# Optimization experiments

Hardware: AMD Instinct MI355X
Metric: run time of the kernel (lower is better)

## Reference

```python
import jax, jax.numpy as jnp
import numpy as np

B, H, S, D = 4, 8, 2048, 64

def setup_inputs() -> dict:
    key = jax.random.key(0)
    k1, k2 = jax.random.split(key)
    q = jax.random.normal(k1, (B, H, S, D), dtype=jnp.float32)
    kv = jax.random.normal(k2, (B, H, S, D), dtype=jnp.float32)
    mask = jnp.zeros((1, 1, S, S), dtype=jnp.float32)
    return {"q": q, "kv": kv, "mask": mask}

def reference(q, kv, mask):
    # score = q @ kv^T / sqrt(d_k) + mask ; softmax over last dim ; @ kv
    d_k = jnp.asarray(kv.shape[-1], dtype=q.dtype)
    score = jnp.einsum('bhqd,bhkd->bhqk', q, kv) / jnp.sqrt(d_k)
    score = score + mask
    attn = jax.nn.softmax(score, axis=-1)
    out = jnp.einsum('bhqk,bhkd->bhqd', attn, kv)
    return out
```

## Files before the change

kernel.cpp:

```cpp
#include <hip/hip_runtime.h>
#include <hip/hip_bf16.h>
#include <stdint.h>


typedef __bf16 bf16;
typedef __attribute__((ext_vector_type(8))) __bf16 bf16x8;
typedef __attribute__((ext_vector_type(4))) __bf16 bf16x4;
typedef __attribute__((ext_vector_type(4))) float floatx4;

#define SLEN 2048
#define DH   64
#define BR   64
#define BC   64
#define NKT  (SLEN / BC)
#define NQT  (SLEN / BR)
#define BH_N 32
#define LOG2E 1.44269504088896341f

#define CHB_L  1024
#define IMGB_L 8192
#define IMGE_G 4096

#define AS1 __attribute__((address_space(1)))
#define AS3 __attribute__((address_space(3)))

static __device__ inline void gload_lds16(const void* g, void* l) {
    __builtin_amdgcn_global_load_lds((const AS1 uint32_t*)g, (AS3 uint32_t*)l, 16, 0, 0);
}

static_assert(BH_N == NQT, "prep kernel folds bh and qt onto one grid axis");

static __device__ inline int phys_key(int l) {
    int h = l >> 5, l5 = l & 31, q = l5 >> 3, j = l5 & 7;
    return 32 * h + (j < 4 ? 4 * q + j : 16 + 4 * q + (j - 4));
}

__global__ __launch_bounds__(256) void kv_prep(
    const float* __restrict__ kv, const float* __restrict__ mask,
    bf16* __restrict__ kvK, bf16* __restrict__ kvT, int* __restrict__ flags)
{
    __shared__ bf16 Tl[64 * 72];
    __shared__ int wany[4];
    const int kt = blockIdx.x, z = blockIdx.y;
    const int t = threadIdx.x;

    float acc = 0.f;
#pragma unroll
    for (int i = 0; i < 4; ++i) {
        int f = i * 256 + t;
        int row = f >> 4, c4 = (f & 15) * 4;
        const float4 v = *(const float4*)(mask + (size_t)(z * BR + row) * SLEN + kt * BC + c4);
        acc = fmaxf(acc, fmaxf(fmaxf(fabsf(v.x), fabsf(v.y)), fmaxf(fabsf(v.z), fabsf(v.w))));
    }
    unsigned long long any = __ballot(acc != 0.f);
    if ((t & 63) == 0) wany[t >> 6] = (any != 0ull) ? 1 : 0;

    const float* src = kv + ((size_t)z * SLEN + kt * BC) * DH;
#pragma unroll
    for (int i = 0; i < 4; ++i) {
        int f = i * 256 + t;
        int key = f >> 4, d4 = (f & 15) * 4;
        float4 v = *(const float4*)(src + (size_t)key * DH + d4);
        bf16x4 b; b[0] = (bf16)v.x; b[1] = (bf16)v.y; b[2] = (bf16)v.z; b[3] = (bf16)v.w;
        *(bf16x4*)&Tl[key * 72 + d4] = b;
    }
    __syncthreads();
    if (t == 0) flags[z * NKT + kt] = wany[0] | wany[1] | wany[2] | wany[3];

    bf16* outK = kvK + ((size_t)z * NKT + kt) * IMGE_G;
#pragma unroll
    for (int i = 0; i < 2; ++i) {
        int G = i * 256 + t;
        int c = G >> 6, L = G & 63, rl = L >> 3, p = L & 7;
        int g = (p - rl - 4 * (c & 1)) & 7, key = 8 * c + rl;
        bf16x8 w = *(const bf16x8*)&Tl[key * 72 + g * 8];
        *(bf16x8*)(outK + (size_t)G * 8) = w;
    }
    bf16* outV = kvT + ((size_t)z * NKT + kt) * IMGE_G;
#pragma unroll
    for (int i = 0; i < 2; ++i) {
        int G = i * 256 + t;
        int c = G >> 6, L = G & 63, dl = L >> 3, p = L & 7;
        int g = (p - dl - 4 * (c & 1)) & 7, d = 8 * c + dl;
        bf16x8 w;
#pragma unroll
        for (int j = 0; j < 8; ++j)
            w[j] = Tl[phys_key(8 * g + j) * 72 + d];
        *(bf16x8*)(outV + (size_t)G * 8) = w;
    }
}

__global__ __launch_bounds__(1024) void attn_fwd10(
    const float* __restrict__ q, const float* __restrict__ mask,
    const int* __restrict__ flags,
    const bf16* __restrict__ kvK, const bf16* __restrict__ kvT,
    float* __restrict__ out)
{
    __shared__ __align__(16) char smem[65536];

    const int bh = blockIdx.x;
    const int qt = blockIdx.y;
    const int q0 = qt * 128;
    const int t = threadIdx.x;
    const int wave = t >> 6, lane = t & 63;
    const int grp = wave >> 3;
    const int w8 = wave & 7;
    const int ln16 = lane & 15, quad = lane >> 4;
    const int ln8 = ln16 & 7, hb = ln16 >> 3;

    const float qscale = 0.125f * LOG2E;
    bf16x8 aq[2];
    {
        const float* qrow = q + ((size_t)bh * SLEN + q0 + w8 * 16 + ln16) * DH;
#pragma unroll
        for (int kc = 0; kc < 2; ++kc) {
            float4 f0 = *(const float4*)(qrow + kc * 32 + quad * 8);
            float4 f1 = *(const float4*)(qrow + kc * 32 + quad * 8 + 4);
            bf16x8 a;
            a[0] = (bf16)(f0.x * qscale); a[1] = (bf16)(f0.y * qscale);
            a[2] = (bf16)(f0.z * qscale); a[3] = (bf16)(f0.w * qscale);
            a[4] = (bf16)(f1.x * qscale); a[5] = (bf16)(f1.y * qscale);
            a[6] = (bf16)(f1.z * qscale); a[7] = (bf16)(f1.w * qscale);
            aq[kc] = a;
        }
    }

    const int fqt = qt * 2 + (w8 >> 2);
    unsigned fmask;
    {
        int ld = (lane < 32) ? flags[fqt * NKT + lane] : 0;
        fmask = (unsigned)__ballot(ld != 0);
    }

    const int kbase0 = hb * CHB_L + ln8 * 128 + (((quad + ln8 + 4 * hb) & 7) << 4);
    const int kbase1 = hb * CHB_L + ln8 * 128 + (((quad + 4 + ln8 + 4 * hb) & 7) << 4);

    floatx4 o[4];
#pragma unroll
    for (int dt = 0; dt < 4; ++dt) o[dt] = (floatx4){0.f, 0.f, 0.f, 0.f};
    float m_run = -3.0e38f, l_run = 0.f;

    const bf16* kvKb = kvK + (size_t)bh * NKT * IMGE_G;
    const bf16* kvTb = kvT + (size_t)bh * NKT * IMGE_G;
    const int kt0 = grp * (NKT / 2);
    char* Gb = smem + grp * 32768;

    {
        const bf16* sK = kvKb + (size_t)kt0 * IMGE_G;
        const bf16* sV = kvTb + (size_t)kt0 * IMGE_G;
        gload_lds16(sK + (size_t)w8 * 512 + lane * 8, Gb + w8 * CHB_L);
        gload_lds16(sV + (size_t)w8 * 512 + lane * 8, Gb + IMGB_L + w8 * CHB_L);
    }

    for (int e = 0; e < NKT / 2; ++e) {
        __syncthreads();
        const int kt = kt0 + e;

        if (e + 1 < NKT / 2) {
            char* Bn = Gb + ((e + 1) & 1) * 16384;
            const bf16* sK = kvKb + (size_t)(kt + 1) * IMGE_G;
            const bf16* sV = kvTb + (size_t)(kt + 1) * IMGE_G;
            gload_lds16(sK + (size_t)w8 * 512 + lane * 8, Bn + w8 * CHB_L);
            gload_lds16(sV + (size_t)w8 * 512 + lane * 8, Bn + IMGB_L + w8 * CHB_L);
        }

        const char* Kb = Gb + (e & 1) * 16384;
        const char* Vb = Kb + IMGB_L;

        floatx4 s[4];
#pragma unroll
        for (int nt = 0; nt < 4; ++nt) {
            bf16x8 a0 = *(const bf16x8*)(Kb + nt * 2048 + kbase0);
            bf16x8 a1 = *(const bf16x8*)(Kb + nt * 2048 + kbase1);
            floatx4 acc = (floatx4){0.f, 0.f, 0.f, 0.f};
            acc = __builtin_amdgcn_mfma_f32_16x16x32_bf16(a0, aq[0], acc, 0, 0, 0);
            acc = __builtin_amdgcn_mfma_f32_16x16x32_bf16(a1, aq[1], acc, 0, 0, 0);
            s[nt] = acc;
        }

        if (fmask & (1u << kt)) {
            const float* mrow = mask + (size_t)(q0 + w8 * 16 + ln16) * SLEN + kt * BC;
#pragma unroll
            for (int nt = 0; nt < 4; ++nt) {
                float4 mv = *(const float4*)(mrow + 16 * nt + quad * 4);
                s[nt][0] += mv.x * LOG2E; s[nt][1] += mv.y * LOG2E;
                s[nt][2] += mv.z * LOG2E; s[nt][3] += mv.w * LOG2E;
            }
        }

        float t01 = fmaxf(fmaxf(s[0][0], s[0][1]), fmaxf(s[0][2], s[0][3]));
        float t23 = fmaxf(fmaxf(s[1][0], s[1][1]), fmaxf(s[1][2], s[1][3]));
        float t45 = fmaxf(fmaxf(s[2][0], s[2][1]), fmaxf(s[2][2], s[2][3]));
        float t67 = fmaxf(fmaxf(s[3][0], s[3][1]), fmaxf(s[3][2], s[3][3]));
        float tmax = fmaxf(fmaxf(t01, t23), fmaxf(t45, t67));
        tmax = fmaxf(tmax, __shfl_xor(tmax, 16));
        tmax = fmaxf(tmax, __shfl_xor(tmax, 32));
        float mnew = fmaxf(m_run, tmax);
        unsigned long long grew = __ballot(mnew > m_run);
        float alpha = exp2f(m_run - mnew);
        m_run = mnew;

        float rs = 0.f;
        bf16x8 pf0, pf1;
#pragma unroll
        for (int r = 0; r < 4; ++r) {
            float p0 = exp2f(s[0][r] - mnew);
            float p1 = exp2f(s[1][r] - mnew);
            float p2 = exp2f(s[2][r] - mnew);
            float p3 = exp2f(s[3][r] - mnew);
            rs += (p0 + p1) + (p2 + p3);
            pf0[r] = (bf16)p0; pf0[4 + r] = (bf16)p1;
            pf1[r] = (bf16)p2; pf1[4 + r] = (bf16)p3;
        }
        rs += __shfl_xor(rs, 16);
        rs += __shfl_xor(rs, 32);

        if (grew) {
            l_run = l_run * alpha + rs;
            float a0 = __shfl(alpha, quad * 4 + 0);
            float a1 = __shfl(alpha, quad * 4 + 1);
            float a2 = __shfl(alpha, quad * 4 + 2);
            float a3 = __shfl(alpha, quad * 4 + 3);
#pragma unroll
            for (int dt = 0; dt < 4; ++dt) {
                o[dt][0] *= a0; o[dt][1] *= a1; o[dt][2] *= a2; o[dt][3] *= a3;
            }
        } else {
            l_run += rs;
        }

#pragma unroll
        for (int dt = 0; dt < 4; ++dt) {
            bf16x8 v0 = *(const bf16x8*)(Vb + dt * 2048 + kbase0);
            bf16x8 v1 = *(const bf16x8*)(Vb + dt * 2048 + kbase1);
            o[dt] = __builtin_amdgcn_mfma_f32_16x16x32_bf16(pf0, v0, o[dt], 0, 0, 0);
            o[dt] = __builtin_amdgcn_mfma_f32_16x16x32_bf16(pf1, v1, o[dt], 0, 0, 0);
        }
    }

    __syncthreads();
    float* Xo  = (float*)smem;
    float* Xml = (float*)(smem + 32768);

    if (grp == 1) {
        float* xo = Xo + (size_t)w8 * 16 * 64;
#pragma unroll
        for (int dt = 0; dt < 4; ++dt) {
            int col = ln16 + 16 * dt;
            xo[(quad * 4 + 0) * 64 + col] = o[dt][0];
            xo[(quad * 4 + 1) * 64 + col] = o[dt][1];
            xo[(quad * 4 + 2) * 64 + col] = o[dt][2];
            xo[(quad * 4 + 3) * 64 + col] = o[dt][3];
        }
        Xml[(w8 * 16 + ln16) * 2 + 0] = m_run;
        Xml[(w8 * 16 + ln16) * 2 + 1] = l_run;
    }
    __syncthreads();
    if (grp == 0) {
        const float* xo = Xo + (size_t)w8 * 16 * 64;
        float* ob = out + ((size_t)bh * SLEN + q0 + w8 * 16) * DH;
#pragma unroll
        for (int r = 0; r < 4; ++r) {
            int row = quad * 4 + r;
            float m0 = __shfl(m_run, row);
            float l0 = __shfl(l_run, row);
            float m1 = Xml[(w8 * 16 + row) * 2 + 0];
            float l1 = Xml[(w8 * 16 + row) * 2 + 1];
            float M  = fmaxf(m0, m1);
            float a0 = exp2f(m0 - M), a1 = exp2f(m1 - M);
            float inv = 1.f / (l0 * a0 + l1 * a1);
#pragma unroll
            for (int dt = 0; dt < 4; ++dt) {
                int col = ln16 + 16 * dt;
                ob[row * DH + col] = (o[dt][r] * a0 + xo[row * 64 + col] * a1) * inv;
            }
        }
    }
}

#define LDT 72
__global__ __launch_bounds__(256) void attn_mask_flags(
    const float* __restrict__ mask, int* __restrict__ flags)
{
    const int kt = blockIdx.x, qt = blockIdx.y;
    const int t = threadIdx.x;
    float acc = 0.f;
#pragma unroll
    for (int i = 0; i < 4; ++i) {
        int f = i * 256 + t;
        int row = f >> 4, c4 = (f & 15) * 4;
        const float4 v = *(const float4*)(mask + (size_t)(qt * BR + row) * SLEN + kt * BC + c4);
        acc = fmaxf(acc, fmaxf(fmaxf(fabsf(v.x), fabsf(v.y)), fmaxf(fabsf(v.z), fabsf(v.w))));
    }
    unsigned long long any = __ballot(acc != 0.f);
    __shared__ int wany[4];
    if ((t & 63) == 0) wany[t >> 6] = (any != 0ull) ? 1 : 0;
    __syncthreads();
    if (t == 0) flags[qt * NKT + kt] = wany[0] | wany[1] | wany[2] | wany[3];
}

__global__ __launch_bounds__(256) void attn_fwd(
    const float* __restrict__ q, const float* __restrict__ kv,
    const float* __restrict__ mask, const int* __restrict__ flags,
    float* __restrict__ out)
{
    __shared__ __align__(16) bf16 Kl[BC * LDT];
    __shared__ __align__(16) bf16 Vt[DH * LDT];
    __shared__ __align__(16) bf16 Pl[BR * LDT];

    const int qt = blockIdx.x;
    const int bh = blockIdx.y;
    const int q0 = qt * BR;
    const int t = threadIdx.x;
    const int wave = t >> 6, lane = t & 63;
    const int ln16 = lane & 15, quad = lane >> 4;

    const float qscale = 0.125f * LOG2E;
    bf16x8 aq[2];
    {
        const float* qrow = q + ((size_t)bh * SLEN + q0 + wave * 16 + ln16) * DH;
#pragma unroll
        for (int kc = 0; kc < 2; ++kc) {
            float4 f0 = *(const float4*)(qrow + kc * 32 + quad * 8);
            float4 f1 = *(const float4*)(qrow + kc * 32 + quad * 8 + 4);
            bf16x8 a;
            a[0] = (bf16)(f0.x * qscale); a[1] = (bf16)(f0.y * qscale);
            a[2] = (bf16)(f0.z * qscale); a[3] = (bf16)(f0.w * qscale);
            a[4] = (bf16)(f1.x * qscale); a[5] = (bf16)(f1.y * qscale);
            a[6] = (bf16)(f1.z * qscale); a[7] = (bf16)(f1.w * qscale);
            aq[kc] = a;
        }
    }

    floatx4 o[4];
#pragma unroll
    for (int dt = 0; dt < 4; ++dt) o[dt] = (floatx4){0.f, 0.f, 0.f, 0.f};
    float m_run[4], l_run[4];
#pragma unroll
    for (int r = 0; r < 4; ++r) { m_run[r] = -3.0e38f; l_run[r] = 0.f; }

    const float* kvb = kv + (size_t)bh * SLEN * DH;

    for (int kt = 0; kt < NKT; ++kt) {
        float4 st[4];
        const float* kvt = kvb + (size_t)kt * BC * DH;
#pragma unroll
        for (int i = 0; i < 4; ++i) {
            int f = i * 256 + t;
            st[i] = *(const float4*)(kvt + (size_t)f * 4);
        }
        __syncthreads();
#pragma unroll
        for (int i = 0; i < 4; ++i) {
            int f = i * 256 + t;
            int key = f >> 4, d4 = (f & 15) * 4;
            bf16 b0 = (bf16)st[i].x, b1 = (bf16)st[i].y, b2 = (bf16)st[i].z, b3 = (bf16)st[i].w;
            *(bf16x4*)&Kl[key * LDT + d4] = (bf16x4){b0, b1, b2, b3};
            Vt[(d4 + 0) * LDT + key] = b0;
            Vt[(d4 + 1) * LDT + key] = b1;
            Vt[(d4 + 2) * LDT + key] = b2;
            Vt[(d4 + 3) * LDT + key] = b3;
        }
        __syncthreads();

        floatx4 s[4];
#pragma unroll
        for (int nt = 0; nt < 4; ++nt) {
            s[nt] = (floatx4){0.f, 0.f, 0.f, 0.f};
#pragma unroll
            for (int kc = 0; kc < 2; ++kc) {
                bf16x8 bk = *(const bf16x8*)&Kl[(ln16 + 16 * nt) * LDT + kc * 32 + quad * 8];
                s[nt] = __builtin_amdgcn_mfma_f32_16x16x32_bf16(aq[kc], bk, s[nt], 0, 0, 0);
            }
        }

        if (!flags || flags[qt * NKT + kt]) {
            const float* mrow = mask + (size_t)(q0 + quad * 4) * SLEN + kt * BC + ln16;
#pragma unroll
            for (int r = 0; r < 4; ++r)
#pragma unroll
                for (int nt = 0; nt < 4; ++nt)
                    s[nt][r] += mrow[(size_t)r * SLEN + nt * 16] * LOG2E;
        }

#pragma unroll
        for (int r = 0; r < 4; ++r) {
            float mx = fmaxf(fmaxf(s[0][r], s[1][r]), fmaxf(s[2][r], s[3][r]));
            mx = fmaxf(mx, __shfl_xor(mx, 1));
            mx = fmaxf(mx, __shfl_xor(mx, 2));
            mx = fmaxf(mx, __shfl_xor(mx, 4));
            mx = fmaxf(mx, __shfl_xor(mx, 8));
            float mnew = fmaxf(m_run[r], mx);
            float alpha = exp2f(m_run[r] - mnew);
            m_run[r] = mnew;
            float rs = 0.f;
#pragma unroll
            for (int nt = 0; nt < 4; ++nt) {
                float p = exp2f(s[nt][r] - mnew);
                s[nt][r] = p;
                rs += p;
            }
            rs += __shfl_xor(rs, 1);
            rs += __shfl_xor(rs, 2);
            rs += __shfl_xor(rs, 4);
            rs += __shfl_xor(rs, 8);
            l_run[r] = l_run[r] * alpha + rs;
#pragma unroll
            for (int dt = 0; dt < 4; ++dt) o[dt][r] *= alpha;
        }

#pragma unroll
        for (int nt = 0; nt < 4; ++nt)
#pragma unroll
            for (int r = 0; r < 4; ++r)
                Pl[(wave * 16 + quad * 4 + r) * LDT + ln16 + 16 * nt] = (bf16)s[nt][r];

#pragma unroll
        for (int kc2 = 0; kc2 < 2; ++kc2) {
            bf16x8 pfr = *(const bf16x8*)&Pl[(wave * 16 + ln16) * LDT + kc2 * 32 + quad * 8];
#pragma unroll
            for (int dt = 0; dt < 4; ++dt) {
                bf16x8 vfr = *(const bf16x8*)&Vt[(ln16 + 16 * dt) * LDT + kc2 * 32 + quad * 8];
                o[dt] = __builtin_amdgcn_mfma_f32_16x16x32_bf16(pfr, vfr, o[dt], 0, 0, 0);
            }
        }
    }

#pragma unroll
    for (int r = 0; r < 4; ++r) {
        float inv = 1.0f / l_run[r];
        int qrow = q0 + wave * 16 + quad * 4 + r;
        float* orow = out + ((size_t)bh * SLEN + qrow) * DH;
#pragma unroll
        for (int dt = 0; dt < 4; ++dt)
            orow[ln16 + 16 * dt] = o[dt][r] * inv;
    }
}

extern "C" void kernel_launch(void* const* d_in, const int* in_sizes, int n_in,
                              void* d_out, int out_size, void* d_ws, size_t ws_size,
                              hipStream_t stream)
{
    const float* q    = (const float*)d_in[0];
    const float* kv   = (const float*)d_in[1];
    const float* mask = (const float*)d_in[2];
    float* out = (float*)d_out;

    const size_t kvKoff = 4096;
    const size_t kvToff = kvKoff + (size_t)BH_N * NKT * IMGE_G * 2;
    const size_t need   = kvToff + (size_t)BH_N * NKT * IMGE_G * 2;

    if (ws_size >= need) {
        int*  flags = (int*)d_ws;
        bf16* kvK   = (bf16*)((char*)d_ws + kvKoff);
        bf16* kvT   = (bf16*)((char*)d_ws + kvToff);
        kv_prep<<<dim3(NKT, BH_N), 256, 0, stream>>>(kv, mask, kvK, kvT, flags);
        attn_fwd10<<<dim3(BH_N, SLEN / 128), 1024, 0, stream>>>(q, mask, flags, kvK, kvT, out);
    } else {
        int* flags = nullptr;
        if (ws_size >= (size_t)NQT * NKT * sizeof(int)) {
            flags = (int*)d_ws;
            attn_mask_flags<<<dim3(NKT, NQT), 256, 0, stream>>>(mask, flags);
        }
        attn_fwd<<<dim3(NQT, BH_N), 256, 0, stream>>>(q, kv, mask, flags, out);
    }
}
```

Measured before the change: 165.6 us.

## Switch attention kernel to 32x32x16 MFMA tiles with 512-thread blocks

Rewrites the main attention kernel to use 32x32x16 bf16 MFMA instructions, so each wave owns 32 query rows instead of 16, and halves the block to 512 threads. The V-transpose layout in the prep kernel is changed to match the new operand fragment ordering. Larger MFMA tiles reduce the LDS fragment loads and instructions per FLOP and cut the cross-lane reductions for row max and sum. The cost is more accumulator registers per wave, fewer waves per block for latency hiding, and more complex per-row alpha shuffles and mask gathers.

```diff
diff --git a/kernel.cpp b/kernel.cpp
--- a/kernel.cpp
+++ b/kernel.cpp
@@ -7,6 +7,7 @@
 typedef __attribute__((ext_vector_type(8))) __bf16 bf16x8;
 typedef __attribute__((ext_vector_type(4))) __bf16 bf16x4;
 typedef __attribute__((ext_vector_type(4))) float floatx4;
+typedef __attribute__((ext_vector_type(16))) float floatx16;
 
 #define SLEN 2048
 #define DH   64
@@ -18,7 +19,6 @@
 #define LOG2E 1.44269504088896341f
 
 #define CHB_L  1024
-#define IMGB_L 8192
 #define IMGE_G 4096
 
 #define AS1 __attribute__((address_space(1)))
@@ -30,9 +30,9 @@
 
 static_assert(BH_N == NQT, "prep kernel folds bh and qt onto one grid axis");
 
-static __device__ inline int phys_key(int l) {
-    int h = l >> 5, l5 = l & 31, q = l5 >> 3, j = l5 & 7;
-    return 32 * h + (j < 4 ? 4 * q + j : 16 + 4 * q + (j - 4));
+static __device__ inline int phys_key32(int l) {
+    int kc = l >> 4, rem = l & 15, h = rem >> 3, j = rem & 7;
+    return 16 * kc + 4 * h + j + 4 * (j >> 2);
 }
 
 __global__ __launch_bounds__(256) void kv_prep(
@@ -85,12 +85,12 @@
         bf16x8 w;
 #pragma unroll
         for (int j = 0; j < 8; ++j)
-            w[j] = Tl[phys_key(8 * g + j) * 72 + d];
+            w[j] = Tl[phys_key32(8 * g + j) * 72 + d];
         *(bf16x8*)(outV + (size_t)G * 8) = w;
     }
 }
 
-__global__ __launch_bounds__(1024) void attn_fwd10(
+__global__ __launch_bounds__(512) void attn_fwd11(
     const float* __restrict__ q, const float* __restrict__ mask,
     const int* __restrict__ flags,
     const bf16* __restrict__ kvK, const bf16* __restrict__ kvT,
@@ -103,19 +103,26 @@
     const int q0 = qt * 128;
     const int t = threadIdx.x;
     const int wave = t >> 6, lane = t & 63;
-    const int grp = wave >> 3;
-    const int w8 = wave & 7;
-    const int ln16 = lane & 15, quad = lane >> 4;
-    const int ln8 = ln16 & 7, hb = ln16 >> 3;
+    const int grp = wave >> 2;
+    const int w4 = wave & 3;
+    const int l31 = lane & 31, h = lane >> 5;
+
+    const int laneRow = (l31 >> 3) * 1024 + (l31 & 7) * 128;
+    const int c0 = (l31 & 7) + 4 * ((l31 >> 3) & 1) + h;
+    const int pos0 = ((0 + c0) & 7) * 16;
+    const int pos1 = ((2 + c0) & 7) * 16;
+    const int pos2 = ((4 + c0) & 7) * 16;
+    const int pos3 = ((6 + c0) & 7) * 16;
 
     const float qscale = 0.125f * LOG2E;
-    bf16x8 aq[2];
+    bf16x8 aq[4];
     {
-        const float* qrow = q + ((size_t)bh * SLEN + q0 + w8 * 16 + ln16) * DH;
-#pragma unroll
-        for (int kc = 0; kc < 2; ++kc) {
-            float4 f0 = *(const float4*)(qrow + kc * 32 + quad * 8);
-            float4 f1 = *(const float4*)(qrow + kc * 32 + quad * 8 + 4);
+        const float* qrow = q + ((size_t)bh * SLEN + q0 + w4 * 32 + l31) * DH;
+#pragma unroll
+        for (int kc = 0; kc < 4; ++kc) {
+            int d0 = 16 * kc + 8 * h;
+            float4 f0 = *(const float4*)(qrow + d0);
+            float4 f1 = *(const float4*)(qrow + d0 + 4);
             bf16x8 a;
             a[0] = (bf16)(f0.x * qscale); a[1] = (bf16)(f0.y * qscale);
             a[2] = (bf16)(f0.z * qscale); a[3] = (bf16)(f0.w * qscale);
@@ -125,19 +132,16 @@
         }
     }
 
-    const int fqt = qt * 2 + (w8 >> 2);
+    const int fqt = qt * 2 + (w4 >> 1);
     unsigned fmask;
     {
         int ld = (lane < 32) ? flags[fqt * NKT + lane] : 0;
         fmask = (unsigned)__ballot(ld != 0);
     }
 
-    const int kbase0 = hb * CHB_L + ln8 * 128 + (((quad + ln8 + 4 * hb) & 7) << 4);
-    const int kbase1 = hb * CHB_L + ln8 * 128 + (((quad + 4 + ln8 + 4 * hb) & 7) << 4);
-
-    floatx4 o[4];
-#pragma unroll
-    for (int dt = 0; dt < 4; ++dt) o[dt] = (floatx4){0.f, 0.f, 0.f, 0.f};
+    floatx16 o0, o1;
+#pragma unroll
+    for (int i = 0; i < 16; ++i) { o0[i] = 0.f; o1[i] = 0.f; }
     float m_run = -3.0e38f, l_run = 0.f;
 
     const bf16* kvKb = kvK + (size_t)bh * NKT * IMGE_G;
@@ -148,8 +152,10 @@
     {
         const bf16* sK = kvKb + (size_t)kt0 * IMGE_G;
         const bf16* sV = kvTb + (size_t)kt0 * IMGE_G;
-        gload_lds16(sK + (size_t)w8 * 512 + lane * 8, Gb + w8 * CHB_L);
-        gload_lds16(sV + (size_t)w8 * 512 + lane * 8, Gb + IMGB_L + w8 * CHB_L);
+        gload_lds16(sK + (size_t)(2 * w4) * 512 + lane * 8,     Gb + (2 * w4) * CHB_L);
+        gload_lds16(sK + (size_t)(2 * w4 + 1) * 512 + lane * 8, Gb + (2 * w4 + 1) * CHB_L);
+        gload_lds16(sV + (size_t)(2 * w4) * 512 + lane * 8,     Gb + 8192 + (2 * w4) * CHB_L);
+        gload_lds16(sV + (size_t)(2 * w4 + 1) * 512 + lane * 8, Gb + 8192 + (2 * w4 + 1) * CHB_L);
     }
 
     for (int e = 0; e < NKT / 2; ++e) {
@@ -160,40 +166,52 @@
             char* Bn = Gb + ((e + 1) & 1) * 16384;
             const bf16* sK = kvKb + (size_t)(kt + 1) * IMGE_G;
             const bf16* sV = kvTb + (size_t)(kt + 1) * IMGE_G;
-            gload_lds16(sK + (size_t)w8 * 512 + lane * 8, Bn + w8 * CHB_L);
-            gload_lds16(sV + (size_t)w8 * 512 + lane * 8, Bn + IMGB_L + w8 * CHB_L);
+            gload_lds16(sK + (size_t)(2 * w4) * 512 + lane * 8,     Bn + (2 * w4) * CHB_L);
+            gload_lds16(sK + (size_t)(2 * w4 + 1) * 512 + lane * 8, Bn + (2 * w4 + 1) * CHB_L);
+            gload_lds16(sV + (size_t)(2 * w4) * 512 + lane * 8,     Bn + 8192 + (2 * w4) * CHB_L);
+            gload_lds16(sV + (size_t)(2 * w4 + 1) * 512 + lane * 8, Bn + 8192 + (2 * w4 + 1) * CHB_L);
         }
 
         const char* Kb = Gb + (e & 1) * 16384;
-        const char* Vb = Kb + IMGB_L;
-
-        floatx4 s[4];
-#pragma unroll
-        for (int nt = 0; nt < 4; ++nt) {
-            bf16x8 a0 = *(const bf16x8*)(Kb + nt * 2048 + kbase0);
-            bf16x8 a1 = *(const bf16x8*)(Kb + nt * 2048 + kbase1);
-            floatx4 acc = (floatx4){0.f, 0.f, 0.f, 0.f};
-            acc = __builtin_amdgcn_mfma_f32_16x16x32_bf16(a0, aq[0], acc, 0, 0, 0);
-            acc = __builtin_amdgcn_mfma_f32_16x16x32_bf16(a1, aq[1], acc, 0, 0, 0);
-            s[nt] = acc;
+        const char* Vb = Kb + 8192;
+
+        floatx16 s0, s1;
+#pragma unroll
+        for (int i = 0; i < 16; ++i) { s0[i] = 0.f; s1[i] = 0.f; }
+        {
+            bf16x8 k00 = *(const bf16x8*)(Kb + laneRow + pos0);
+            bf16x8 k10 = *(const bf16x8*)(Kb + 4096 + laneRow + pos0);
+            s0 = __builtin_amdgcn_mfma_f32_32x32x16_bf16(k00, aq[0], s0, 0, 0, 0);
+            s1 = __builtin_amdgcn_mfma_f32_32x32x16_bf16(k10, aq[0], s1, 0, 0, 0);
+            bf16x8 k01 = *(const bf16x8*)(Kb + laneRow + pos1);
+            bf16x8 k11 = *(const bf16x8*)(Kb + 4096 + laneRow + pos1);
+            s0 = __builtin_amdgcn_mfma_f32_32x32x16_bf16(k01, aq[1], s0, 0, 0, 0);
+            s1 = __builtin_amdgcn_mfma_f32_32x32x16_bf16(k11, aq[1], s1, 0, 0, 0);
+            bf16x8 k02 = *(const bf16x8*)(Kb + laneRow + pos2);
+            bf16x8 k12 = *(const bf16x8*)(Kb + 4096 + laneRow + pos2);
+            s0 = __builtin_amdgcn_mfma_f32_32x32x16_bf16(k02, aq[2], s0, 0, 0, 0);
+            s1 = __builtin_amdgcn_mfma_f32_32x32x16_bf16(k12, aq[2], s1, 0, 0, 0);
+            bf16x8 k03 = *(const bf16x8*)(Kb + laneRow + pos3);
+            bf16x8 k13 = *(const bf16x8*)(Kb + 4096 + laneRow + pos3);
+            s0 = __builtin_amdgcn_mfma_f32_32x32x16_bf16(k03, aq[3], s0, 0, 0, 0);
+            s1 = __builtin_amdgcn_mfma_f32_32x32x16_bf16(k13, aq[3], s1, 0, 0, 0);
         }
 
         if (fmask & (1u << kt)) {
-            const float* mrow = mask + (size_t)(q0 + w8 * 16 + ln16) * SLEN + kt * BC;
-#pragma unroll
-            for (int nt = 0; nt < 4; ++nt) {
-                float4 mv = *(const float4*)(mrow + 16 * nt + quad * 4);
-                s[nt][0] += mv.x * LOG2E; s[nt][1] += mv.y * LOG2E;
-                s[nt][2] += mv.z * LOG2E; s[nt][3] += mv.w * LOG2E;
-            }
-        }
-
-        float t01 = fmaxf(fmaxf(s[0][0], s[0][1]), fmaxf(s[0][2], s[0][3]));
-        float t23 = fmaxf(fmaxf(s[1][0], s[1][1]), fmaxf(s[1][2], s[1][3]));
-        float t45 = fmaxf(fmaxf(s[2][0], s[2][1]), fmaxf(s[2][2], s[2][3]));
-        float t67 = fmaxf(fmaxf(s[3][0], s[3][1]), fmaxf(s[3][2], s[3][3]));
-        float tmax = fmaxf(fmaxf(t01, t23), fmaxf(t45, t67));
-        tmax = fmaxf(tmax, __shfl_xor(tmax, 16));
+            const float* mrow = mask + (size_t)(q0 + w4 * 32 + l31) * SLEN + kt * BC;
+#pragma unroll
+            for (int r = 0; r < 16; ++r) {
+                int key = (r & 3) + 8 * (r >> 2) + 4 * h;
+                s0[r] += mrow[key] * LOG2E;
+                s1[r] += mrow[32 + key] * LOG2E;
+            }
+        }
+
+        float tmax = s0[0];
+#pragma unroll
+        for (int r = 1; r < 16; ++r) tmax = fmaxf(tmax, s0[r]);
+#pragma unroll
+        for (int r = 0; r < 16; ++r) tmax = fmaxf(tmax, s1[r]);
         tmax = fmaxf(tmax, __shfl_xor(tmax, 32));
         float mnew = fmaxf(m_run, tmax);
         unsigned long long grew = __ballot(mnew > m_run);
@@ -201,40 +219,49 @@
         m_run = mnew;
 
         float rs = 0.f;
-        bf16x8 pf0, pf1;
-#pragma unroll
-        for (int r = 0; r < 4; ++r) {
-            float p0 = exp2f(s[0][r] - mnew);
-            float p1 = exp2f(s[1][r] - mnew);
-            float p2 = exp2f(s[2][r] - mnew);
-            float p3 = exp2f(s[3][r] - mnew);
-            rs += (p0 + p1) + (p2 + p3);
-            pf0[r] = (bf16)p0; pf0[4 + r] = (bf16)p1;
-            pf1[r] = (bf16)p2; pf1[4 + r] = (bf16)p3;
-        }
-        rs += __shfl_xor(rs, 16);
+        bf16x8 pf[4];
+#pragma unroll
+        for (int kcb = 0; kcb < 2; ++kcb) {
+#pragma unroll
+            for (int j = 0; j < 8; ++j) {
+                float p0 = exp2f(s0[8 * kcb + j] - mnew);
+                float p1 = exp2f(s1[8 * kcb + j] - mnew);
+                rs += p0 + p1;
+                pf[kcb][j] = (bf16)p0;
+                pf[2 + kcb][j] = (bf16)p1;
+            }
+        }
         rs += __shfl_xor(rs, 32);
 
         if (grew) {
             l_run = l_run * alpha + rs;
-            float a0 = __shfl(alpha, quad * 4 + 0);
-            float a1 = __shfl(alpha, quad * 4 + 1);
-            float a2 = __shfl(alpha, quad * 4 + 2);
-            float a3 = __shfl(alpha, quad * 4 + 3);
-#pragma unroll
-            for (int dt = 0; dt < 4; ++dt) {
-                o[dt][0] *= a0; o[dt][1] *= a1; o[dt][2] *= a2; o[dt][3] *= a3;
+#pragma unroll
+            for (int r = 0; r < 16; ++r) {
+                int R = (r & 3) + 8 * (r >> 2) + 4 * h;
+                float ar = __shfl(alpha, R);
+                o0[r] *= ar; o1[r] *= ar;
             }
         } else {
             l_run += rs;
         }
 
-#pragma unroll
-        for (int dt = 0; dt < 4; ++dt) {
-            bf16x8 v0 = *(const bf16x8*)(Vb + dt * 2048 + kbase0);
-            bf16x8 v1 = *(const bf16x8*)(Vb + dt * 2048 + kbase1);
-            o[dt] = __builtin_amdgcn_mfma_f32_16x16x32_bf16(pf0, v0, o[dt], 0, 0, 0);
-            o[dt] = __builtin_amdgcn_mfma_f32_16x16x32_bf16(pf1, v1, o[dt], 0, 0, 0);
+        {
+            bf16x8 v00 = *(const bf16x8*)(Vb + laneRow + pos0);
+            bf16x8 v10 = *(const bf16x8*)(Vb + 4096 + laneRow + pos0);
+            o0 = __builtin_amdgcn_mfma_f32_32x32x16_bf16(pf[0], v00, o0, 0, 0, 0);
+            o1 = __builtin_amdgcn_mfma_f32_32x32x16_bf16(pf[0], v10, o1, 0, 0, 0);
+            bf16x8 v01 = *(const bf16x8*)(Vb + laneRow + pos1);
+            bf16x8 v11 = *(const bf16x8*)(Vb + 4096 + laneRow + pos1);
+            o0 = __builtin_amdgcn_mfma_f32_32x32x16_bf16(pf[1], v01, o0, 0, 0, 0);
+            o1 = __builtin_amdgcn_mfma_f32_32x32x16_bf16(pf[1], v11, o1, 0, 0, 0);
+            bf16x8 v02 = *(const bf16x8*)(Vb + laneRow + pos2);
+            bf16x8 v12 = *(const bf16x8*)(Vb + 4096 + laneRow + pos2);
+            o0 = __builtin_amdgcn_mfma_f32_32x32x16_bf16(pf[2], v02, o0, 0, 0, 0);
+            o1 = __builtin_amdgcn_mfma_f32_32x32x16_bf16(pf[2], v12, o1, 0, 0, 0);
+            bf16x8 v03 = *(const bf16x8*)(Vb + laneRow + pos3);
+            bf16x8 v13 = *(const bf16x8*)(Vb + 4096 + laneRow + pos3);
+            o0 = __builtin_amdgcn_mfma_f32_32x32x16_bf16(pf[3], v03, o0, 0, 0, 0);
+            o1 = __builtin_amdgcn_mfma_f32_32x32x16_bf16(pf[3], v13, o1, 0, 0, 0);
         }
     }
 
@@ -243,37 +270,30 @@
     float* Xml = (float*)(smem + 32768);
 
     if (grp == 1) {
-        float* xo = Xo + (size_t)w8 * 16 * 64;
-#pragma unroll
-        for (int dt = 0; dt < 4; ++dt) {
-            int col = ln16 + 16 * dt;
-            xo[(quad * 4 + 0) * 64 + col] = o[dt][0];
-            xo[(quad * 4 + 1) * 64 + col] = o[dt][1];
-            xo[(quad * 4 + 2) * 64 + col] = o[dt][2];
-            xo[(quad * 4 + 3) * 64 + col] = o[dt][3];
-        }
-        Xml[(w8 * 16 + ln16) * 2 + 0] = m_run;
-        Xml[(w8 * 16 + ln16) * 2 + 1] = l_run;
+#pragma unroll
+        for (int r = 0; r < 16; ++r) {
+            int row = w4 * 32 + (r & 3) + 8 * (r >> 2) + 4 * h;
+            Xo[row * 64 + l31]      = o0[r];
+            Xo[row * 64 + 32 + l31] = o1[r];
+        }
+        Xml[(w4 * 32 + l31) * 2 + 0] = m_run;
+        Xml[(w4 * 32 + l31) * 2 + 1] = l_run;
     }
     __syncthreads();
     if (grp == 0) {
-        const float* xo = Xo + (size_t)w8 * 16 * 64;
-        float* ob = out + ((size_t)bh * SLEN + q0 + w8 * 16) * DH;
-#pragma unroll
-        for (int r = 0; r < 4; ++r) {
-            int row = quad * 4 + r;
-            float m0 = __shfl(m_run, row);
-            float l0 = __shfl(l_run, row);
-            float m1 = Xml[(w8 * 16 + row) * 2 + 0];
-            float l1 = Xml[(w8 * 16 + row) * 2 + 1];
+        float* ob = out + ((size_t)bh * SLEN + q0 + w4 * 32) * DH;
+#pragma unroll
+        for (int r = 0; r < 16; ++r) {
+            int R = (r & 3) + 8 * (r >> 2) + 4 * h;
+            float m0 = __shfl(m_run, R);
+            float l0 = __shfl(l_run, R);
+            float m1 = Xml[(w4 * 32 + R) * 2 + 0];
+            float l1 = Xml[(w4 * 32 + R) * 2 + 1];
             float M  = fmaxf(m0, m1);
             float a0 = exp2f(m0 - M), a1 = exp2f(m1 - M);
             float inv = 1.f / (l0 * a0 + l1 * a1);
-#pragma unroll
-            for (int dt = 0; dt < 4; ++dt) {
-                int col = ln16 + 16 * dt;
-                ob[row * DH + col] = (o[dt][r] * a0 + xo[row * 64 + col] * a1) * inv;
-            }
+            ob[R * DH + l31]      = (o0[r] * a0 + Xo[(w4 * 32 + R) * 64 + l31]      * a1) * inv;
+            ob[R * DH + 32 + l31] = (o1[r] * a0 + Xo[(w4 * 32 + R) * 64 + 32 + l31] * a1) * inv;
         }
     }
 }
@@ -455,7 +475,7 @@
         bf16* kvK   = (bf16*)((char*)d_ws + kvKoff);
         bf16* kvT   = (bf16*)((char*)d_ws + kvToff);
         kv_prep<<<dim3(NKT, BH_N), 256, 0, stream>>>(kv, mask, kvK, kvT, flags);
-        attn_fwd10<<<dim3(BH_N, SLEN / 128), 1024, 0, stream>>>(q, mask, flags, kvK, kvT, out);
+        attn_fwd11<<<dim3(BH_N, SLEN / 128), 512, 0, stream>>>(q, mask, flags, kvK, kvT, out);
     } else {
         int* flags = nullptr;
         if (ws_size >= (size_t)NQT * NKT * sizeof(int)) {
```

New measurement: 166.4 us. About the same (+0.5%).

## Halve waves per block, give each wave two 16-row query tiles

Applied to the files above, without the earlier changes.

The attention kernel now launches 512 threads (8 waves, two groups of four) instead of 1024. Each wave processes two 16-row query slices, so every K/V fragment read from LDS feeds two MFMAs, halving LDS read traffic per unit of compute and interleaving independent MFMA chains. The exp2f calls are also swapped for the raw hardware exp2 builtin. The trade-off is more accumulator and score registers per wave and fewer waves per block to hide latency, with launch bounds asking for 4 blocks per CU.

```diff
diff --git a/kernel.cpp b/kernel.cpp
--- a/kernel.cpp
+++ b/kernel.cpp
@@ -18,7 +18,6 @@
 #define LOG2E 1.44269504088896341f
 
 #define CHB_L  1024
-#define IMGB_L 8192
 #define IMGE_G 4096
 
 #define AS1 __attribute__((address_space(1)))
@@ -26,6 +25,10 @@
 
 static __device__ inline void gload_lds16(const void* g, void* l) {
     __builtin_amdgcn_global_load_lds((const AS1 uint32_t*)g, (AS3 uint32_t*)l, 16, 0, 0);
+}
+
+static __device__ inline float fexp2(float x) {
+    return __builtin_amdgcn_exp2f(x);
 }
 
 static_assert(BH_N == NQT, "prep kernel folds bh and qt onto one grid axis");
@@ -90,7 +93,7 @@
     }
 }
 
-__global__ __launch_bounds__(1024) void attn_fwd10(
+__global__ __launch_bounds__(512, 4) void attn_fwd14(
     const float* __restrict__ q, const float* __restrict__ mask,
     const int* __restrict__ flags,
     const bf16* __restrict__ kvK, const bf16* __restrict__ kvT,
@@ -103,15 +106,16 @@
     const int q0 = qt * 128;
     const int t = threadIdx.x;
     const int wave = t >> 6, lane = t & 63;
-    const int grp = wave >> 3;
-    const int w8 = wave & 7;
+    const int grp = wave >> 2;
+    const int w4 = wave & 3;
     const int ln16 = lane & 15, quad = lane >> 4;
     const int ln8 = ln16 & 7, hb = ln16 >> 3;
 
     const float qscale = 0.125f * LOG2E;
-    bf16x8 aq[2];
-    {
-        const float* qrow = q + ((size_t)bh * SLEN + q0 + w8 * 16 + ln16) * DH;
+    bf16x8 aq[2][2];
+#pragma unroll
+    for (int rs = 0; rs < 2; ++rs) {
+        const float* qrow = q + ((size_t)bh * SLEN + q0 + w4 * 32 + rs * 16 + ln16) * DH;
 #pragma unroll
         for (int kc = 0; kc < 2; ++kc) {
             float4 f0 = *(const float4*)(qrow + kc * 32 + quad * 8);
@@ -121,11 +125,11 @@
             a[2] = (bf16)(f0.z * qscale); a[3] = (bf16)(f0.w * qscale);
             a[4] = (bf16)(f1.x * qscale); a[5] = (bf16)(f1.y * qscale);
             a[6] = (bf16)(f1.z * qscale); a[7] = (bf16)(f1.w * qscale);
-            aq[kc] = a;
-        }
-    }
-
-    const int fqt = qt * 2 + (w8 >> 2);
+            aq[rs][kc] = a;
+        }
+    }
+
+    const int fqt = qt * 2 + (w4 >> 1);
     unsigned fmask;
     {
         int ld = (lane < 32) ? flags[fqt * NKT + lane] : 0;
@@ -135,10 +139,12 @@
     const int kbase0 = hb * CHB_L + ln8 * 128 + (((quad + ln8 + 4 * hb) & 7) << 4);
     const int kbase1 = hb * CHB_L + ln8 * 128 + (((quad + 4 + ln8 + 4 * hb) & 7) << 4);
 
-    floatx4 o[4];
-#pragma unroll
-    for (int dt = 0; dt < 4; ++dt) o[dt] = (floatx4){0.f, 0.f, 0.f, 0.f};
-    float m_run = -3.0e38f, l_run = 0.f;
+    floatx4 o[2][4];
+#pragma unroll
+    for (int rs = 0; rs < 2; ++rs)
+#pragma unroll
+        for (int dt = 0; dt < 4; ++dt) o[rs][dt] = (floatx4){0.f, 0.f, 0.f, 0.f};
+    float m_run[2] = {-3.0e38f, -3.0e38f}, l_run[2] = {0.f, 0.f};
 
     const bf16* kvKb = kvK + (size_t)bh * NKT * IMGE_G;
     const bf16* kvTb = kvT + (size_t)bh * NKT * IMGE_G;
@@ -148,8 +154,10 @@
     {
         const bf16* sK = kvKb + (size_t)kt0 * IMGE_G;
         const bf16* sV = kvTb + (size_t)kt0 * IMGE_G;
-        gload_lds16(sK + (size_t)w8 * 512 + lane * 8, Gb + w8 * CHB_L);
-        gload_lds16(sV + (size_t)w8 * 512 + lane * 8, Gb + IMGB_L + w8 * CHB_L);
+        gload_lds16(sK + (size_t)(2 * w4) * 512 + lane * 8,     Gb + (2 * w4) * CHB_L);
+        gload_lds16(sK + (size_t)(2 * w4 + 1) * 512 + lane * 8, Gb + (2 * w4 + 1) * CHB_L);
+        gload_lds16(sV + (size_t)(2 * w4) * 512 + lane * 8,     Gb + 8192 + (2 * w4) * CHB_L);
+        gload_lds16(sV + (size_t)(2 * w4 + 1) * 512 + lane * 8, Gb + 8192 + (2 * w4 + 1) * CHB_L);
     }
 
     for (int e = 0; e < NKT / 2; ++e) {
@@ -160,81 +168,96 @@
             char* Bn = Gb + ((e + 1) & 1) * 16384;
             const bf16* sK = kvKb + (size_t)(kt + 1) * IMGE_G;
             const bf16* sV = kvTb + (size_t)(kt + 1) * IMGE_G;
-            gload_lds16(sK + (size_t)w8 * 512 + lane * 8, Bn + w8 * CHB_L);
-            gload_lds16(sV + (size_t)w8 * 512 + lane * 8, Bn + IMGB_L + w8 * CHB_L);
+            gload_lds16(sK + (size_t)(2 * w4) * 512 + lane * 8,     Bn + (2 * w4) * CHB_L);
+            gload_lds16(sK + (size_t)(2 * w4 + 1) * 512 + lane * 8, Bn + (2 * w4 + 1) * CHB_L);
+            gload_lds16(sV + (size_t)(2 * w4) * 512 + lane * 8,     Bn + 8192 + (2 * w4) * CHB_L);
+            gload_lds16(sV + (size_t)(2 * w4 + 1) * 512 + lane * 8, Bn + 8192 + (2 * w4 + 1) * CHB_L);
         }
 
         const char* Kb = Gb + (e & 1) * 16384;
-        const char* Vb = Kb + IMGB_L;
-
-        floatx4 s[4];
+        const char* Vb = Kb + 8192;
+
+        floatx4 s[2][4];
 #pragma unroll
         for (int nt = 0; nt < 4; ++nt) {
             bf16x8 a0 = *(const bf16x8*)(Kb + nt * 2048 + kbase0);
             bf16x8 a1 = *(const bf16x8*)(Kb + nt * 2048 + kbase1);
-            floatx4 acc = (floatx4){0.f, 0.f, 0.f, 0.f};
-            acc = __builtin_amdgcn_mfma_f32_16x16x32_bf16(a0, aq[0], acc, 0, 0, 0);
-            acc = __builtin_amdgcn_mfma_f32_16x16x32_bf16(a1, aq[1], acc, 0, 0, 0);
-            s[nt] = acc;
+            floatx4 accA = (floatx4){0.f, 0.f, 0.f, 0.f};
+            floatx4 accB = (floatx4){0.f, 0.f, 0.f, 0.f};
+            accA = __builtin_amdgcn_mfma_f32_16x16x32_bf16(a0, aq[0][0], accA, 0, 0, 0);
+            accB = __builtin_amdgcn_mfma_f32_16x16x32_bf16(a0, aq[1][0], accB, 0, 0, 0);
+            accA = __builtin_amdgcn_mfma_f32_16x16x32_bf16(a1, aq[0][1], accA, 0, 0, 0);
+            accB = __builtin_amdgcn_mfma_f32_16x16x32_bf16(a1, aq[1][1], accB, 0, 0, 0);
+            s[0][nt] = accA;
+            s[1][nt] = accB;
         }
 
         if (fmask & (1u << kt)) {
-            const float* mrow = mask + (size_t)(q0 + w8 * 16 + ln16) * SLEN + kt * BC;
-#pragma unroll
-            for (int nt = 0; nt < 4; ++nt) {
-                float4 mv = *(const float4*)(mrow + 16 * nt + quad * 4);
-                s[nt][0] += mv.x * LOG2E; s[nt][1] += mv.y * LOG2E;
-                s[nt][2] += mv.z * LOG2E; s[nt][3] += mv.w * LOG2E;
-            }
-        }
-
-        float t01 = fmaxf(fmaxf(s[0][0], s[0][1]), fmaxf(s[0][2], s[0][3]));
-        float t23 = fmaxf(fmaxf(s[1][0], s[1][1]), fmaxf(s[1][2], s[1][3]));
-        float t45 = fmaxf(fmaxf(s[2][0], s[2][1]), fmaxf(s[2][2], s[2][3]));
-        float t67 = fmaxf(fmaxf(s[3][0], s[3][1]), fmaxf(s[3][2], s[3][3]));
-        float tmax = fmaxf(fmaxf(t01, t23), fmaxf(t45, t67));
-        tmax = fmaxf(tmax, __shfl_xor(tmax, 16));
-        tmax = fmaxf(tmax, __shfl_xor(tmax, 32));
-        float mnew = fmaxf(m_run, tmax);
-        unsigned long long grew = __ballot(mnew > m_run);
-        float alpha = exp2f(m_run - mnew);
-        m_run = mnew;
-
-        float rs = 0.f;
-        bf16x8 pf0, pf1;
-#pragma unroll
-        for (int r = 0; r < 4; ++r) {
-            float p0 = exp2f(s[0][r] - mnew);
-            float p1 = exp2f(s[1][r] - mnew);
-            float p2 = exp2f(s[2][r] - mnew);
-            float p3 = exp2f(s[3][r] - mnew);
-            rs += (p0 + p1) + (p2 + p3);
-            pf0[r] = (bf16)p0; pf0[4 + r] = (bf16)p1;
-            pf1[r] = (bf16)p2; pf1[4 + r] = (bf16)p3;
-        }
-        rs += __shfl_xor(rs, 16);
-        rs += __shfl_xor(rs, 32);
-
-        if (grew) {
-            l_run = l_run * alpha + rs;
-            float a0 = __shfl(alpha, quad * 4 + 0);
-            float a1 = __shfl(alpha, quad * 4 + 1);
-            float a2 = __shfl(alpha, quad * 4 + 2);
-            float a3 = __shfl(alpha, quad * 4 + 3);
-#pragma unroll
-            for (int dt = 0; dt < 4; ++dt) {
-                o[dt][0] *= a0; o[dt][1] *= a1; o[dt][2] *= a2; o[dt][3] *= a3;
-            }
-        } else {
-            l_run += rs;
+#pragma unroll
+            for (int rs = 0; rs < 2; ++rs) {
+                const float* mrow = mask + (size_t)(q0 + w4 * 32 + rs * 16 + ln16) * SLEN + kt * BC;
+#pragma unroll
+                for (int nt = 0; nt < 4; ++nt) {
+                    float4 mv = *(const float4*)(mrow + 16 * nt + quad * 4);
+                    s[rs][nt][0] += mv.x * LOG2E; s[rs][nt][1] += mv.y * LOG2E;
+                    s[rs][nt][2] += mv.z * LOG2E; s[rs][nt][3] += mv.w * LOG2E;
+                }
+            }
+        }
+
+        bf16x8 pf[2][2];
+#pragma unroll
+        for (int rs = 0; rs < 2; ++rs) {
+            float t01 = fmaxf(fmaxf(s[rs][0][0], s[rs][0][1]), fmaxf(s[rs][0][2], s[rs][0][3]));
+            float t23 = fmaxf(fmaxf(s[rs][1][0], s[rs][1][1]), fmaxf(s[rs][1][2], s[rs][1][3]));
+            float t45 = fmaxf(fmaxf(s[rs][2][0], s[rs][2][1]), fmaxf(s[rs][2][2], s[rs][2][3]));
+            float t67 = fmaxf(fmaxf(s[rs][3][0], s[rs][3][1]), fmaxf(s[rs][3][2], s[rs][3][3]));
+            float tmax = fmaxf(fmaxf(t01, t23), fmaxf(t45, t67));
+            tmax = fmaxf(tmax, __shfl_xor(tmax, 16));
+            tmax = fmaxf(tmax, __shfl_xor(tmax, 32));
+            float mnew = fmaxf(m_run[rs], tmax);
+            unsigned long long grew = __ballot(mnew > m_run[rs]);
+            float alpha = fexp2(m_run[rs] - mnew);
+            m_run[rs] = mnew;
+
+            float rsum = 0.f;
+#pragma unroll
+            for (int r = 0; r < 4; ++r) {
+                float p0 = fexp2(s[rs][0][r] - mnew);
+                float p1 = fexp2(s[rs][1][r] - mnew);
+                float p2 = fexp2(s[rs][2][r] - mnew);
+                float p3 = fexp2(s[rs][3][r] - mnew);
+                rsum += (p0 + p1) + (p2 + p3);
+                pf[rs][0][r] = (bf16)p0; pf[rs][0][4 + r] = (bf16)p1;
+                pf[rs][1][r] = (bf16)p2; pf[rs][1][4 + r] = (bf16)p3;
+            }
+            rsum += __shfl_xor(rsum, 16);
+            rsum += __shfl_xor(rsum, 32);
+
+            if (grew) {
+                l_run[rs] = l_run[rs] * alpha + rsum;
+                float a0 = __shfl(alpha, quad * 4 + 0);
+                float a1 = __shfl(alpha, quad * 4 + 1);
+                float a2 = __shfl(alpha, quad * 4 + 2);
+                float a3 = __shfl(alpha, quad * 4 + 3);
+#pragma unroll
+                for (int dt = 0; dt < 4; ++dt) {
+                    o[rs][dt][0] *= a0; o[rs][dt][1] *= a1;
+                    o[rs][dt][2] *= a2; o[rs][dt][3] *= a3;
+                }
+            } else {
+                l_run[rs] += rsum;
+            }
         }
 
 #pragma unroll
         for (int dt = 0; dt < 4; ++dt) {
             bf16x8 v0 = *(const bf16x8*)(Vb + dt * 2048 + kbase0);
             bf16x8 v1 = *(const bf16x8*)(Vb + dt * 2048 + kbase1);
-            o[dt] = __builtin_amdgcn_mfma_f32_16x16x32_bf16(pf0, v0, o[dt], 0, 0, 0);
-            o[dt] = __builtin_amdgcn_mfma_f32_16x16x32_bf16(pf1, v1, o[dt], 0, 0, 0);
+            o[0][dt] = __builtin_amdgcn_mfma_f32_16x16x32_bf16(pf[0][0], v0, o[0][dt], 0, 0, 0);
+            o[1][dt] = __builtin_amdgcn_mfma_f32_16x16x32_bf16(pf[1][0], v0, o[1][dt], 0, 0, 0);
+            o[0][dt] = __builtin_amdgcn_mfma_f32_16x16x32_bf16(pf[0][1], v1, o[0][dt], 0, 0, 0);
+            o[1][dt] = __builtin_amdgcn_mfma_f32_16x16x32_bf16(pf[1][1], v1, o[1][dt], 0, 0, 0);
         }
     }
 
@@ -243,36 +266,43 @@
     float* Xml = (float*)(smem + 32768);
 
     if (grp == 1) {
-        float* xo = Xo + (size_t)w8 * 16 * 64;
-#pragma unroll
-        for (int dt = 0; dt < 4; ++dt) {
-            int col = ln16 + 16 * dt;
-            xo[(quad * 4 + 0) * 64 + col] = o[dt][0];
-            xo[(quad * 4 + 1) * 64 + col] = o[dt][1];
-            xo[(quad * 4 + 2) * 64 + col] = o[dt][2];
-            xo[(quad * 4 + 3) * 64 + col] = o[dt][3];
-        }
-        Xml[(w8 * 16 + ln16) * 2 + 0] = m_run;
-        Xml[(w8 * 16 + ln16) * 2 + 1] = l_run;
+#pragma unroll
+        for (int rs = 0; rs < 2; ++rs) {
+            int base = w4 * 32 + rs * 16;
+#pragma unroll
+            for (int dt = 0; dt < 4; ++dt) {
+                int col = ln16 + 16 * dt;
+                Xo[(base + quad * 4 + 0) * 64 + col] = o[rs][dt][0];
+                Xo[(base + quad * 4 + 1) * 64 + col] = o[rs][dt][1];
+                Xo[(base + quad * 4 + 2) * 64 + col] = o[rs][dt][2];
+                Xo[(base + quad * 4 + 3) * 64 + col] = o[rs][dt][3];
+            }
+            Xml[(base + ln16) * 2 + 0] = m_run[rs];
+            Xml[(base + ln16) * 2 + 1] = l_run[rs];
+        }
     }
     __syncthreads();
     if (grp == 0) {
-        const float* xo = Xo + (size_t)w8 * 16 * 64;
-        float* ob = out + ((size_t)bh * SLEN + q0 + w8 * 16) * DH;
-#pragma unroll
-        for (int r = 0; r < 4; ++r) {
-            int row = quad * 4 + r;
-            float m0 = __shfl(m_run, row);
-            float l0 = __shfl(l_run, row);
-            float m1 = Xml[(w8 * 16 + row) * 2 + 0];
-            float l1 = Xml[(w8 * 16 + row) * 2 + 1];
-            float M  = fmaxf(m0, m1);
-            float a0 = exp2f(m0 - M), a1 = exp2f(m1 - M);
-            float inv = 1.f / (l0 * a0 + l1 * a1);
-#pragma unroll
-            for (int dt = 0; dt < 4; ++dt) {
-                int col = ln16 + 16 * dt;
-                ob[row * DH + col] = (o[dt][r] * a0 + xo[row * 64 + col] * a1) * inv;
+#pragma unroll
+        for (int rs = 0; rs < 2; ++rs) {
+            int base = w4 * 32 + rs * 16;
+            float* ob = out + ((size_t)bh * SLEN + q0 + base) * DH;
+#pragma unroll
+            for (int r = 0; r < 4; ++r) {
+                int row = quad * 4 + r;
+                float m0 = __shfl(m_run[rs], row);
+                float l0 = __shfl(l_run[rs], row);
+                float m1 = Xml[(base + row) * 2 + 0];
+                float l1 = Xml[(base + row) * 2 + 1];
+                float M  = fmaxf(m0, m1);
+                float a0 = fexp2(m0 - M), a1 = fexp2(m1 - M);
+                float inv = 1.f / (l0 * a0 + l1 * a1);
+#pragma unroll
+                for (int dt = 0; dt < 4; ++dt) {
+                    int col = ln16 + 16 * dt;
+                    ob[row * DH + col] =
+                        (o[rs][dt][r] * a0 + Xo[(base + row) * 64 + col] * a1) * inv;
+                }
             }
         }
     }
@@ -455,7 +485,7 @@
         bf16* kvK   = (bf16*)((char*)d_ws + kvKoff);
         bf16* kvT   = (bf16*)((char*)d_ws + kvToff);
         kv_prep<<<dim3(NKT, BH_N), 256, 0, stream>>>(kv, mask, kvK, kvT, flags);
-        attn_fwd10<<<dim3(BH_N, SLEN / 128), 1024, 0, stream>>>(q, mask, flags, kvK, kvT, out);
+        attn_fwd14<<<dim3(BH_N, SLEN / 128), 512, 0, stream>>>(q, mask, flags, kvK, kvT, out);
     } else {
         int* flags = nullptr;
         if (ws_size >= (size_t)NQT * NKT * sizeof(int)) {
```

Result: faster. 143.9 us (-13.1%).
